# Performance work log

Measured on AMD Instinct MI355X. Metric: run time of the kernel, lower is better.

Reference implementation:

```python
import jax, jax.numpy as jnp
import numpy as np

VAR0, VAR1 = 0.1, 0.2          # SSD variances
IOU_THRESH = 0.5
NUM_CLASSES = 21
NEGPOS_RATIO = 3
ALPHA = 1.0


def mid_to_corner(b):
    # [cx,cy,w,h] -> [xmin,ymin,xmax,ymax]
    return jnp.concatenate([b[:, :2] - b[:, 2:] / 2, b[:, :2] + b[:, 2:] / 2], axis=1)


def jaccard(box_a, box_b):
    # box_a [n,4], box_b [P,4] corner form -> IoU [n,P]
    lt = jnp.maximum(box_a[:, None, :2], box_b[None, :, :2])
    rb = jnp.minimum(box_a[:, None, 2:], box_b[None, :, 2:])
    wh = jnp.clip(rb - lt, 0.0)
    inter = wh[..., 0] * wh[..., 1]
    area_a = (box_a[:, 2] - box_a[:, 0]) * (box_a[:, 3] - box_a[:, 1])
    area_b = (box_b[:, 2] - box_b[:, 0]) * (box_b[:, 3] - box_b[:, 1])
    union = area_a[:, None] + area_b[None, :] - inter
    return inter / union


def encode_offset(matched, priors):
    # matched corner form [P,4], priors center form [P,4]
    g_cxcy = ((matched[:, :2] + matched[:, 2:]) / 2 - priors[:, :2]) / (VAR0 * priors[:, 2:])
    g_wh = jnp.log((matched[:, 2:] - matched[:, :2]) / priors[:, 2:]) / VAR1
    return jnp.concatenate([g_cxcy, g_wh], axis=1)


def match_one(gt_box, gt_cls, valid, priors_corner, priors_mid):
    # gt_box [n,4], gt_cls [n], valid [n] bool; priors [P,4]
    n = gt_box.shape[0]
    P = priors_corner.shape[0]
    ovl = jaccard(gt_box, priors_corner)                    # [n,P]
    ovl = jnp.where(valid[:, None], ovl, -1.0)              # mask padded GTs
    best_truth_idx = jnp.argmax(ovl, axis=0)                # [P]
    best_truth_ovl = jnp.max(ovl, axis=0)                   # [P]
    best_prior_idx = jnp.argmax(ovl, axis=1)                # [n]
    bpi = jnp.where(valid, best_prior_idx, P)               # OOB for padded -> dropped
    best_truth_ovl = best_truth_ovl.at[bpi].set(2.0, mode='drop')
    best_truth_idx = best_truth_idx.at[bpi].set(jnp.arange(n), mode='drop')
    matches = gt_box[best_truth_idx]                        # [P,4]
    loc = encode_offset(matches, priors_mid)                # [P,4]
    conf = gt_cls[best_truth_idx].astype(jnp.int32) + 1     # [P]
    conf = jnp.where(best_truth_ovl < IOU_THRESH, 0, conf)
    return loc, conf


def setup_inputs() -> dict:
    key = jax.random.key(0)
    k = jax.random.split(key, 8)
    B, P, C, NMAX = 64, 8732, 21, 50
    confidence = jax.random.normal(k[0], (B, P, C), dtype=jnp.float32)
    location = 0.1 * jax.random.normal(k[1], (B, P, 4), dtype=jnp.float32)
    cxcy = jax.random.uniform(k[2], (P, 2), minval=0.05, maxval=0.95)
    pwh = jax.random.uniform(k[3], (P, 2), minval=0.05, maxval=0.4)
    prior_boxes = jnp.concatenate([cxcy, pwh], axis=1).astype(jnp.float32)
    xymin = jax.random.uniform(k[4], (B, NMAX, 2), minval=0.0, maxval=0.6)
    gwh = jax.random.uniform(k[5], (B, NMAX, 2), minval=0.05, maxval=0.35)
    cls = jax.random.randint(k[6], (B, NMAX), 0, C - 1).astype(jnp.float32)
    labels = jnp.concatenate([xymin, xymin + gwh, cls[..., None]], axis=-1).astype(jnp.float32)
    obj_count = jax.random.randint(k[7], (B, 1), 1, NMAX + 1).astype(jnp.int32)
    return {"confidence": confidence, "location": location,
            "prior_boxes": prior_boxes, "labels": labels, "obj_count": obj_count}


def reference(confidence, location, prior_boxes, labels, obj_count):
    B, P, C = confidence.shape
    NMAX = labels.shape[1]
    priors_corner = mid_to_corner(prior_boxes)
    valid = jnp.arange(NMAX)[None, :] < obj_count            # [B,NMAX]
    loc_t, conf_t = jax.vmap(match_one, in_axes=(0, 0, 0, None, None))(
        labels[..., :4], labels[..., 4], valid, priors_corner, prior_boxes)
    # loc_t [B,P,4] float, conf_t [B,P] int32

    pos = conf_t > 0                                          # [B,P]
    # smooth-L1 over positive anchors (sum reduction)
    d = jnp.abs(location - loc_t)
    sl1 = jnp.where(d < 1.0, 0.5 * d * d, d - 0.5)
    loss_loc = jnp.sum(sl1 * pos[..., None].astype(sl1.dtype))

    # hard negative mining score: global-max logsumexp minus target logit
    bc = confidence.reshape(-1, C)
    x_max = jnp.max(bc)
    lse = jnp.log(jnp.sum(jnp.exp(bc - x_max), axis=1)) + x_max
    tgt_logit = jnp.take_along_axis(bc, conf_t.reshape(-1, 1), axis=1)[:, 0]
    loss_c = (lse - tgt_logit).reshape(B, P)
    loss_c = jnp.where(pos, 0.0, loss_c)
    loss_idx = jnp.argsort(-loss_c, axis=1)                   # descending sort
    idx_rank = jnp.argsort(loss_idx, axis=1)
    num_pos = jnp.sum(pos.astype(jnp.int32), axis=1, keepdims=True)   # [B,1]
    num_neg = jnp.clip(NEGPOS_RATIO * num_pos, None, P - 1)
    neg = idx_rank < num_neg                                  # [B,P]

    # standard cross entropy over selected (pos|neg) anchors, sum reduction
    logp = jax.nn.log_softmax(confidence, axis=-1)            # [B,P,C]
    nll = -jnp.take_along_axis(logp, conf_t[..., None], axis=-1)[..., 0]
    sel = jnp.logical_or(pos, neg)
    loss_conf = jnp.sum(nll * sel.astype(nll.dtype))

    N = jnp.sum(num_pos).astype(confidence.dtype)
    return (ALPHA * loss_loc / N, loss_conf / N)
```

## Files before the change

### kernel.cpp

```cpp
#include <hip/hip_runtime.h>
#include <math.h>

#define Bn 64
#define Pn 8732
#define Cn 21
#define NMAXn 50
#define PX 35

template <int C>
__device__ __forceinline__ float dppf(float x) {
    return __int_as_float(__builtin_amdgcn_update_dpp(0, __float_as_int(x), C, 0xf, 0xf, true));
}
template <int C>
__device__ __forceinline__ int dppi(int x) {
    return __builtin_amdgcn_update_dpp(0, x, C, 0xf, 0xf, true);
}
__device__ __forceinline__ float wave_sum_f(float x) {
    x += dppf<0x111>(x); x += dppf<0x112>(x); x += dppf<0x114>(x);
    x += dppf<0x118>(x); x += dppf<0x142>(x); x += dppf<0x143>(x);
    return x;
}
__device__ __forceinline__ int wave_sum_i(int x) {
    x += dppi<0x111>(x); x += dppi<0x112>(x); x += dppi<0x114>(x);
    x += dppi<0x118>(x); x += dppi<0x142>(x); x += dppi<0x143>(x);
    return x;
}

__device__ __forceinline__ float smoothl1_enc(const float4 l, const float4 pr,
                                              float gx0, float gy0, float gx1, float gy1) {
    const float tx = ((gx0 + gx1) * 0.5f - pr.x) / (0.1f * pr.z);
    const float ty = ((gy0 + gy1) * 0.5f - pr.y) / (0.1f * pr.w);
    const float tw = __logf((gx1 - gx0) / pr.z) * 5.0f;
    const float th = __logf((gy1 - gy0) / pr.w) * 5.0f;
    float s = 0.0f, d;
    d = fabsf(l.x - tx); s += (d < 1.0f) ? 0.5f * d * d : d - 0.5f;
    d = fabsf(l.y - ty); s += (d < 1.0f) ? 0.5f * d * d : d - 0.5f;
    d = fabsf(l.z - tw); s += (d < 1.0f) ? 0.5f * d * d : d - 0.5f;
    d = fabsf(l.w - th); s += (d < 1.0f) ? 0.5f * d * d : d - 0.5f;
    return s;
}

__global__ __launch_bounds__(256) void k_fused(const float* __restrict__ conf,
                                               const float* __restrict__ loc,
                                               const float* __restrict__ priors,
                                               const float* __restrict__ labels,
                                               const int* __restrict__ objc,
                                               float* __restrict__ lc,
                                               float* __restrict__ part_loc,
                                               float* __restrict__ part_nll,
                                               int* __restrict__ part_np,
                                               int* __restrict__ sbp_g) {
    const int bx = blockIdx.x;
    const int tid = threadIdx.x;
    const int lane = tid & 63, wid = tid >> 6;

    __shared__ float sconf[256 * Cn];
    __shared__ float lab[NMAXn * 5];
    __shared__ float rl[4], rn[4];
    __shared__ int rp[4];
    __shared__ float wkI[4], wkU[4];
    __shared__ int wkP[4];

    if (bx < Bn * PX) {
        const int b = bx / PX;
        const int px = bx % PX;
        const int p0 = px * 256;
        const int rows = min(256, Pn - p0);
        const int cnt = objc[b];
        const float* lb = labels + b * NMAXn * 5;

        const float4* src = reinterpret_cast<const float4*>(conf + ((size_t)b * Pn + p0) * Cn);
        const int n4 = rows * Cn / 4;
        for (int i = tid; i < n4; i += 256) reinterpret_cast<float4*>(sconf)[i] = src[i];
        for (int i = tid; i < NMAXn * 5; i += 256) lab[i] = labels[b * NMAXn * 5 + i];

        const int p = p0 + tid;
        const int pcl = (p < Pn) ? p : (Pn - 1);
        const float4 pr = reinterpret_cast<const float4*>(priors)[pcl];
        const float px0 = pr.x - 0.5f * pr.z, py0 = pr.y - 0.5f * pr.w;
        const float px1 = pr.x + 0.5f * pr.z, py1 = pr.y + 0.5f * pr.w;
        const float parea = (px1 - px0) * (py1 - py0);
        float bI = 0.0f, bU = 1.0f;
        int bidx = 0;
        {
            const float gx0 = lb[0], gy0 = lb[1], gx1 = lb[2], gy1 = lb[3];
            const float lx = fmaxf(gx0, px0), ly = fmaxf(gy0, py0);
            const float rx = fminf(gx1, px1), ry = fminf(gy1, py1);
            const float w = fmaxf(rx - lx, 0.0f), h = fmaxf(ry - ly, 0.0f);
            bI = w * h;
            bU = (gx1 - gx0) * (gy1 - gy0) + parea - bI;
        }
        for (int n = 1; n < cnt; ++n) {
            const float gx0 = lb[n * 5 + 0], gy0 = lb[n * 5 + 1];
            const float gx1 = lb[n * 5 + 2], gy1 = lb[n * 5 + 3];
            const float lx = fmaxf(gx0, px0), ly = fmaxf(gy0, py0);
            const float rx = fminf(gx1, px1), ry = fminf(gy1, py1);
            const float w = fmaxf(rx - lx, 0.0f), h = fmaxf(ry - ly, 0.0f);
            const float I = w * h;
            const float U = (gx1 - gx0) * (gy1 - gy0) + parea - I;
            if (I * bU > bI * U) { bI = I; bU = U; bidx = n; }
        }
        __syncthreads();

        float my_loc = 0.0f, my_nll = 0.0f;
        int my_np = 0;
        if (tid < rows) {
            const size_t gi = (size_t)b * Pn + p;
            const int ct = (2.0f * bI >= bU) ? ((int)lab[bidx * 5 + 4] + 1) : 0;
            const float* row = sconf + tid * Cn;
            float m = row[0];
#pragma unroll
            for (int j = 1; j < Cn; ++j) m = fmaxf(m, row[j]);
            float s2 = 0.0f;
#pragma unroll
            for (int j = 0; j < Cn; ++j) s2 += __expf(row[j] - m);
            const float nll = __logf(s2) + m - row[ct];
            if (ct > 0) {
                lc[gi] = 0.0f;
                my_np = 1;
                my_nll = nll;
                const float4 l = reinterpret_cast<const float4*>(loc)[gi];
                my_loc = smoothl1_enc(l, pr, lab[bidx * 5 + 0], lab[bidx * 5 + 1],
                                      lab[bidx * 5 + 2], lab[bidx * 5 + 3]);
            } else {
                lc[gi] = nll;
            }
        }
        my_loc = wave_sum_f(my_loc);
        my_nll = wave_sum_f(my_nll);
        my_np = wave_sum_i(my_np);
        if (lane == 63) { rl[wid] = my_loc; rn[wid] = my_nll; rp[wid] = my_np; }
        __syncthreads();
        if (tid == 0) {
            const int g = b * PX + px;
            part_loc[g] = rl[0] + rl[1] + rl[2] + rl[3];
            part_nll[g] = rn[0] + rn[1] + rn[2] + rn[3];
            part_np[g] = rp[0] + rp[1] + rp[2] + rp[3];
        }
    } else {
        const int idx = bx - Bn * PX;
        const int b = idx / NMAXn;
        const int n = idx % NMAXn;
        if (n >= objc[b]) return;
        const float* lbp = labels + (b * NMAXn + n) * 5;
        const float gx0 = lbp[0], gy0 = lbp[1], gx1 = lbp[2], gy1 = lbp[3];
        const float ga = (gx1 - gx0) * (gy1 - gy0);
        float bI, bU;
        int bp_;
        {
            const float4 pr = reinterpret_cast<const float4*>(priors)[tid];
            const float px0 = pr.x - 0.5f * pr.z, py0 = pr.y - 0.5f * pr.w;
            const float px1 = pr.x + 0.5f * pr.z, py1 = pr.y + 0.5f * pr.w;
            const float lx = fmaxf(gx0, px0), ly = fmaxf(gy0, py0);
            const float rx = fminf(gx1, px1), ry = fminf(gy1, py1);
            const float w = fmaxf(rx - lx, 0.0f), h = fmaxf(ry - ly, 0.0f);
            bI = w * h;
            bU = ga + (px1 - px0) * (py1 - py0) - bI;
            bp_ = tid;
        }
        for (int j = 1; j < PX; ++j) {
            const int p = tid + 256 * j;
            if (p < Pn) {
                const float4 pr = reinterpret_cast<const float4*>(priors)[p];
                const float px0 = pr.x - 0.5f * pr.z, py0 = pr.y - 0.5f * pr.w;
                const float px1 = pr.x + 0.5f * pr.z, py1 = pr.y + 0.5f * pr.w;
                const float lx = fmaxf(gx0, px0), ly = fmaxf(gy0, py0);
                const float rx = fminf(gx1, px1), ry = fminf(gy1, py1);
                const float w = fmaxf(rx - lx, 0.0f), h = fmaxf(ry - ly, 0.0f);
                const float I = w * h;
                const float U = ga + (px1 - px0) * (py1 - py0) - I;
                if (I * bU > bI * U) { bI = I; bU = U; bp_ = p; }
            }
        }
        for (int off = 32; off > 0; off >>= 1) {
            const float oI = __shfl_down(bI, off);
            const float oU = __shfl_down(bU, off);
            const int op = __shfl_down(bp_, off);
            const float a = oI * bU, c = bI * oU;
            if (a > c || (a == c && op < bp_)) { bI = oI; bU = oU; bp_ = op; }
        }
        if (lane == 0) { wkI[wid] = bI; wkU[wid] = bU; wkP[wid] = bp_; }
        __syncthreads();
        if (tid == 0) {
            float cI = wkI[0], cU = wkU[0];
            int cp = wkP[0];
#pragma unroll
            for (int w = 1; w < 4; ++w) {
                const float a = wkI[w] * cU, c = cI * wkU[w];
                if (a > c || (a == c && wkP[w] < cp)) { cI = wkI[w]; cU = wkU[w]; cp = wkP[w]; }
            }
            sbp_g[b * NMAXn + n] = cp;
        }
    }
}

__global__ __launch_bounds__(64) void k_fix(const float* __restrict__ conf,
                                            const float* __restrict__ loc,
                                            const float* __restrict__ priors,
                                            const float* __restrict__ labels,
                                            const int* __restrict__ objc,
                                            const int* __restrict__ sbp_g,
                                            float* __restrict__ lc,
                                            int* __restrict__ fix_np,
                                            float* __restrict__ fix_nll,
                                            float* __restrict__ fix_loc,
                                            int* __restrict__ done) {
    __shared__ int sbp[NMAXn];
    __shared__ float lab[NMAXn * 5];
    const int b = blockIdx.x;
    const int tid = threadIdx.x;
    if (b == 0 && tid == 0) *done = 0;
    const int cnt = objc[b];
    for (int i = tid; i < NMAXn * 5; i += 64) lab[i] = labels[b * NMAXn * 5 + i];
    if (tid < cnt) sbp[tid] = sbp_g[b * NMAXn + tid];
    __syncthreads();
    bool win = false;
    if (tid < cnt) {
        const int myp = sbp[tid];
        win = true;
        for (int n2 = tid + 1; n2 < cnt; ++n2) win = win && (sbp[n2] != myp);
    }
    float dnll = 0.0f, dloc = 0.0f;
    int dnp = 0;
    if (win) {
        const int pp = sbp[tid];
        const float4 prf = reinterpret_cast<const float4*>(priors)[pp];
        const float qx0 = prf.x - 0.5f * prf.z, qy0 = prf.y - 0.5f * prf.w;
        const float qx1 = prf.x + 0.5f * prf.z, qy1 = prf.y + 0.5f * prf.w;
        const float qarea = (qx1 - qx0) * (qy1 - qy0);
        float bI = 0.0f, bU = 1.0f;
        int bidx2 = 0;
        {
            const float gx0 = lab[0], gy0 = lab[1], gx1 = lab[2], gy1 = lab[3];
            const float lx = fmaxf(gx0, qx0), ly = fmaxf(gy0, qy0);
            const float rx = fminf(gx1, qx1), ry = fminf(gy1, qy1);
            const float w = fmaxf(rx - lx, 0.0f), h = fmaxf(ry - ly, 0.0f);
            bI = w * h;
            bU = (gx1 - gx0) * (gy1 - gy0) + qarea - bI;
        }
        for (int n2 = 1; n2 < cnt; ++n2) {
            const float gx0 = lab[n2 * 5 + 0], gy0 = lab[n2 * 5 + 1];
            const float gx1 = lab[n2 * 5 + 2], gy1 = lab[n2 * 5 + 3];
            const float lx = fmaxf(gx0, qx0), ly = fmaxf(gy0, qy0);
            const float rx = fminf(gx1, qx1), ry = fminf(gy1, qy1);
            const float w = fmaxf(rx - lx, 0.0f), h = fmaxf(ry - ly, 0.0f);
            const float I = w * h;
            const float U = (gx1 - gx0) * (gy1 - gy0) + qarea - I;
            if (I * bU > bI * U) { bI = I; bU = U; bidx2 = n2; }
        }
        const float* rowg = conf + ((size_t)b * Pn + pp) * Cn;
        float m2 = rowg[0];
#pragma unroll
        for (int j = 1; j < Cn; ++j) m2 = fmaxf(m2, rowg[j]);
        float ss = 0.0f;
#pragma unroll
        for (int j = 0; j < Cn; ++j) ss += __expf(rowg[j] - m2);
        const float lse = __logf(ss) + m2;
        const int ctn = (int)lab[tid * 5 + 4] + 1;
        const float4 lv = reinterpret_cast<const float4*>(loc)[(size_t)b * Pn + pp];
        dnll = lse - rowg[ctn];
        dloc = smoothl1_enc(lv, prf, lab[tid * 5 + 0], lab[tid * 5 + 1],
                            lab[tid * 5 + 2], lab[tid * 5 + 3]);
        dnp = 1;
        if (2.0f * bI >= bU) {
            const int cto = (int)lab[bidx2 * 5 + 4] + 1;
            dnll -= (lse - rowg[cto]);
            dloc -= smoothl1_enc(lv, prf, lab[bidx2 * 5 + 0], lab[bidx2 * 5 + 1],
                                 lab[bidx2 * 5 + 2], lab[bidx2 * 5 + 3]);
            dnp = 0;
        }
        lc[(size_t)b * Pn + pp] = 0.0f;
    }
    dnll = wave_sum_f(dnll);
    dloc = wave_sum_f(dloc);
    dnp = wave_sum_i(dnp);
    if (tid == 63) {
        fix_nll[b] = dnll;
        fix_loc[b] = dloc;
        fix_np[b] = dnp;
    }
}

__global__ __launch_bounds__(256) void k_neg(const float* __restrict__ lc,
                                             const float* __restrict__ part_loc,
                                             const float* __restrict__ part_nll,
                                             const int* __restrict__ part_np,
                                             const int* __restrict__ fix_np,
                                             const float* __restrict__ fix_nll,
                                             const float* __restrict__ fix_loc,
                                             float* __restrict__ negsum,
                                             int* __restrict__ done,
                                             float* __restrict__ out) {
    const int b = blockIdx.x;
    const int tid = threadIdx.x;
    const int lane = tid & 63, wid = tid >> 6;
    __shared__ int redc[2][4];
    __shared__ float redf[4], redf2[4];
    __shared__ int redi[4];
    __shared__ int np_sh, islast;

    const int NV = Pn / 4;
    const float4* src = reinterpret_cast<const float4*>(lc + (size_t)b * Pn);
    const float4 sent = make_float4(-1.0f, -1.0f, -1.0f, -1.0f);
    float4 rr[12];
#pragma unroll
    for (int j = 0; j < 12; ++j) {
        const int i = tid + 256 * j;
        rr[j] = (i < NV) ? src[i] : sent;
    }

    if (tid < 64) {
        int npl = (tid < PX) ? part_np[b * PX + tid] : 0;
        npl = wave_sum_i(npl);
        if (tid == 63) np_sh = npl;
    }
    __syncthreads();
    const int k = min(3 * (np_sh + fix_np[b]), Pn - 1);

    unsigned lo = 0u, hi = 0x7F800000u;
#pragma unroll 1
    for (int it = 0; it < 31; ++it) {
        const unsigned mid = lo + ((hi - lo) >> 1);
        const float fm = __uint_as_float(mid);
        int c = 0;
#pragma unroll
        for (int j = 0; j < 12; ++j)
            c += (rr[j].x >= fm) + (rr[j].y >= fm) + (rr[j].z >= fm) + (rr[j].w >= fm);
        c = wave_sum_i(c);
        if (lane == 63) redc[it & 1][wid] = c;
        __syncthreads();
        const int tot = redc[it & 1][0] + redc[it & 1][1]
                      + redc[it & 1][2] + redc[it & 1][3];
        if (tot >= k) lo = mid;
        else hi = mid;
    }
    const float v = __uint_as_float(lo);

    float sm = 0.0f;
    int c = 0;
#pragma unroll
    for (int j = 0; j < 12; ++j) {
        if (rr[j].x > v) { sm += rr[j].x; ++c; }
        if (rr[j].y > v) { sm += rr[j].y; ++c; }
        if (rr[j].z > v) { sm += rr[j].z; ++c; }
        if (rr[j].w > v) { sm += rr[j].w; ++c; }
    }
    sm = wave_sum_f(sm);
    c = wave_sum_i(c);
    if (lane == 63) { redf[wid] = sm; redi[wid] = c; }
    __syncthreads();
    if (tid == 0) {
        const float st = redf[0] + redf[1] + redf[2] + redf[3];
        const int ct = redi[0] + redi[1] + redi[2] + redi[3];
        negsum[b] = st + (float)(k - ct) * v;
        __threadfence();
        islast = (atomicAdd(done, 1) == Bn - 1) ? 1 : 0;
    }
    __syncthreads();
    if (!islast) return;
    __threadfence();

    float sl = 0.0f, sn = 0.0f;
    int np = 0;
    for (int i = tid; i < Bn * PX; i += 256) {
        sl += part_loc[i];
        sn += part_nll[i];
        np += part_np[i];
    }
    if (tid < Bn) {
        sn += negsum[tid] + fix_nll[tid];
        sl += fix_loc[tid];
        np += fix_np[tid];
    }
    sl = wave_sum_f(sl);
    sn = wave_sum_f(sn);
    np = wave_sum_i(np);
    if (lane == 63) { redf[wid] = sn; redf2[wid] = sl; redi[wid] = np; }
    __syncthreads();
    if (tid == 0) {
        const float fN = (float)(redi[0] + redi[1] + redi[2] + redi[3]);
        out[0] = (redf2[0] + redf2[1] + redf2[2] + redf2[3]) / fN;
        out[1] = (redf[0] + redf[1] + redf[2] + redf[3]) / fN;
    }
}

extern "C" void kernel_launch(void* const* d_in, const int* in_sizes, int n_in,
                              void* d_out, int out_size, void* d_ws, size_t ws_size,
                              hipStream_t stream) {
    const float* conf = (const float*)d_in[0];
    const float* loc = (const float*)d_in[1];
    const float* priors = (const float*)d_in[2];
    const float* labels = (const float*)d_in[3];
    const int* objc = (const int*)d_in[4];
    float* out = (float*)d_out;

    int* sbp_g = (int*)d_ws;
    float* part_loc = (float*)(sbp_g + Bn * NMAXn);
    float* part_nll = part_loc + Bn * PX;
    int* part_np = (int*)(part_nll + Bn * PX);
    float* negsum = (float*)(part_np + Bn * PX);
    int* fix_np = (int*)(negsum + Bn);
    float* fix_nll = (float*)(fix_np + Bn);
    float* fix_loc = fix_nll + Bn;
    float* lc = fix_loc + Bn;
    int* done = (int*)(lc + (size_t)Bn * Pn);

    k_fused<<<Bn * PX + Bn * NMAXn, 256, 0, stream>>>(conf, loc, priors, labels, objc,
                                                      lc, part_loc, part_nll, part_np,
                                                      sbp_g);
    k_fix<<<Bn, 64, 0, stream>>>(conf, loc, priors, labels, objc, sbp_g, lc,
                                 fix_np, fix_nll, fix_loc, done);
    k_neg<<<Bn, 256, 0, stream>>>(lc, part_loc, part_nll, part_np,
                                  fix_np, fix_nll, fix_loc, negsum, done, out);
}
```

Measured before the change: 70.29 us.

## Fuse forced-match fixup into negative-mining kernel and dual-accumulate IoU argmax loops

Removes the separate k_fix launch by running the forced-match correction inside the negative-mining kernel. The corrected prior indices are applied to register-held loss values instead of being written back to global memory. Both IoU argmax loops in the main kernel now keep two independent running maxima to shorten the dependency chain, then merge them with an index tie-break. The done-counter reset moves into the first kernel. This saves one launch and a global round trip, but adds serial fixup work before the bisection in each block.

```diff
diff --git a/kernel.cpp b/kernel.cpp
--- a/kernel.cpp
+++ b/kernel.cpp
@@ -40,6 +40,15 @@
     return s;
 }
 
+#define IOU_IU(gx0, gy0, gx1, gy1, qx0, qy0, qx1, qy1, qarea, I, U)            \
+    {                                                                          \
+        const float lx = fmaxf(gx0, qx0), ly = fmaxf(gy0, qy0);                \
+        const float rx = fminf(gx1, qx1), ry = fminf(gy1, qy1);                \
+        const float w = fmaxf(rx - lx, 0.0f), h = fmaxf(ry - ly, 0.0f);        \
+        I = w * h;                                                             \
+        U = (gx1 - gx0) * (gy1 - gy0) + qarea - I;                             \
+    }
+
 __global__ __launch_bounds__(256) void k_fused(const float* __restrict__ conf,
                                                const float* __restrict__ loc,
                                                const float* __restrict__ priors,
@@ -49,10 +58,12 @@
                                                float* __restrict__ part_loc,
                                                float* __restrict__ part_nll,
                                                int* __restrict__ part_np,
-                                               int* __restrict__ sbp_g) {
+                                               int* __restrict__ sbp_g,
+                                               int* __restrict__ done) {
     const int bx = blockIdx.x;
     const int tid = threadIdx.x;
     const int lane = tid & 63, wid = tid >> 6;
+    if (bx == 0 && tid == 0) *done = 0;
 
     __shared__ float sconf[256 * Cn];
     __shared__ float lab[NMAXn * 5];
@@ -80,25 +91,27 @@
         const float px0 = pr.x - 0.5f * pr.z, py0 = pr.y - 0.5f * pr.w;
         const float px1 = pr.x + 0.5f * pr.z, py1 = pr.y + 0.5f * pr.w;
         const float parea = (px1 - px0) * (py1 - py0);
-        float bI = 0.0f, bU = 1.0f;
-        int bidx = 0;
+        float bI0 = 0.0f, bU0 = 1.0f, bI1 = 0.0f, bU1 = 1.0f;
+        int bx0 = 0, bx1 = 0;
+        int n = 0;
+        for (; n + 1 < cnt; n += 2) {
+            float I0, U0, I1, U1;
+            IOU_IU(lb[n * 5 + 0], lb[n * 5 + 1], lb[n * 5 + 2], lb[n * 5 + 3],
+                   px0, py0, px1, py1, parea, I0, U0);
+            IOU_IU(lb[(n + 1) * 5 + 0], lb[(n + 1) * 5 + 1], lb[(n + 1) * 5 + 2],
+                   lb[(n + 1) * 5 + 3], px0, py0, px1, py1, parea, I1, U1);
+            if (I0 * bU0 > bI0 * U0) { bI0 = I0; bU0 = U0; bx0 = n; }
+            if (I1 * bU1 > bI1 * U1) { bI1 = I1; bU1 = U1; bx1 = n + 1; }
+        }
+        if (n < cnt) {
+            float I0, U0;
+            IOU_IU(lb[n * 5 + 0], lb[n * 5 + 1], lb[n * 5 + 2], lb[n * 5 + 3],
+                   px0, py0, px1, py1, parea, I0, U0);
+            if (I0 * bU0 > bI0 * U0) { bI0 = I0; bU0 = U0; bx0 = n; }
+        }
         {
-            const float gx0 = lb[0], gy0 = lb[1], gx1 = lb[2], gy1 = lb[3];
-            const float lx = fmaxf(gx0, px0), ly = fmaxf(gy0, py0);
-            const float rx = fminf(gx1, px1), ry = fminf(gy1, py1);
-            const float w = fmaxf(rx - lx, 0.0f), h = fmaxf(ry - ly, 0.0f);
-            bI = w * h;
-            bU = (gx1 - gx0) * (gy1 - gy0) + parea - bI;
-        }
-        for (int n = 1; n < cnt; ++n) {
-            const float gx0 = lb[n * 5 + 0], gy0 = lb[n * 5 + 1];
-            const float gx1 = lb[n * 5 + 2], gy1 = lb[n * 5 + 3];
-            const float lx = fmaxf(gx0, px0), ly = fmaxf(gy0, py0);
-            const float rx = fminf(gx1, px1), ry = fminf(gy1, py1);
-            const float w = fmaxf(rx - lx, 0.0f), h = fmaxf(ry - ly, 0.0f);
-            const float I = w * h;
-            const float U = (gx1 - gx0) * (gy1 - gy0) + parea - I;
-            if (I * bU > bI * U) { bI = I; bU = U; bidx = n; }
+            const float a = bI1 * bU0, c = bI0 * bU1;
+            if (a > c || (a == c && bx1 < bx0)) { bI0 = bI1; bU0 = bU1; bx0 = bx1; }
         }
         __syncthreads();
 
@@ -106,7 +119,7 @@
         int my_np = 0;
         if (tid < rows) {
             const size_t gi = (size_t)b * Pn + p;
-            const int ct = (2.0f * bI >= bU) ? ((int)lab[bidx * 5 + 4] + 1) : 0;
+            const int ct = (2.0f * bI0 >= bU0) ? ((int)lab[bx0 * 5 + 4] + 1) : 0;
             const float* row = sconf + tid * Cn;
             float m = row[0];
 #pragma unroll
@@ -120,8 +133,8 @@
                 my_np = 1;
                 my_nll = nll;
                 const float4 l = reinterpret_cast<const float4*>(loc)[gi];
-                my_loc = smoothl1_enc(l, pr, lab[bidx * 5 + 0], lab[bidx * 5 + 1],
-                                      lab[bidx * 5 + 2], lab[bidx * 5 + 3]);
+                my_loc = smoothl1_enc(l, pr, lab[bx0 * 5 + 0], lab[bx0 * 5 + 1],
+                                      lab[bx0 * 5 + 2], lab[bx0 * 5 + 3]);
             } else {
                 lc[gi] = nll;
             }
@@ -144,42 +157,69 @@
         if (n >= objc[b]) return;
         const float* lbp = labels + (b * NMAXn + n) * 5;
         const float gx0 = lbp[0], gy0 = lbp[1], gx1 = lbp[2], gy1 = lbp[3];
-        const float ga = (gx1 - gx0) * (gy1 - gy0);
-        float bI, bU;
-        int bp_;
+        float bI0, bU0, bI1, bU1;
+        int bp0, bp1;
         {
             const float4 pr = reinterpret_cast<const float4*>(priors)[tid];
-            const float px0 = pr.x - 0.5f * pr.z, py0 = pr.y - 0.5f * pr.w;
-            const float px1 = pr.x + 0.5f * pr.z, py1 = pr.y + 0.5f * pr.w;
-            const float lx = fmaxf(gx0, px0), ly = fmaxf(gy0, py0);
-            const float rx = fminf(gx1, px1), ry = fminf(gy1, py1);
-            const float w = fmaxf(rx - lx, 0.0f), h = fmaxf(ry - ly, 0.0f);
-            bI = w * h;
-            bU = ga + (px1 - px0) * (py1 - py0) - bI;
-            bp_ = tid;
-        }
-        for (int j = 1; j < PX; ++j) {
-            const int p = tid + 256 * j;
-            if (p < Pn) {
-                const float4 pr = reinterpret_cast<const float4*>(priors)[p];
-                const float px0 = pr.x - 0.5f * pr.z, py0 = pr.y - 0.5f * pr.w;
-                const float px1 = pr.x + 0.5f * pr.z, py1 = pr.y + 0.5f * pr.w;
-                const float lx = fmaxf(gx0, px0), ly = fmaxf(gy0, py0);
-                const float rx = fminf(gx1, px1), ry = fminf(gy1, py1);
-                const float w = fmaxf(rx - lx, 0.0f), h = fmaxf(ry - ly, 0.0f);
-                const float I = w * h;
-                const float U = ga + (px1 - px0) * (py1 - py0) - I;
-                if (I * bU > bI * U) { bI = I; bU = U; bp_ = p; }
-            }
+            const float qx0 = pr.x - 0.5f * pr.z, qy0 = pr.y - 0.5f * pr.w;
+            const float qx1 = pr.x + 0.5f * pr.z, qy1 = pr.y + 0.5f * pr.w;
+            IOU_IU(gx0, gy0, gx1, gy1, qx0, qy0, qx1, qy1,
+                   (qx1 - qx0) * (qy1 - qy0), bI0, bU0);
+            bp0 = tid;
+        }
+        {
+            const float4 pr = reinterpret_cast<const float4*>(priors)[tid + 256];
+            const float qx0 = pr.x - 0.5f * pr.z, qy0 = pr.y - 0.5f * pr.w;
+            const float qx1 = pr.x + 0.5f * pr.z, qy1 = pr.y + 0.5f * pr.w;
+            IOU_IU(gx0, gy0, gx1, gy1, qx0, qy0, qx1, qy1,
+                   (qx1 - qx0) * (qy1 - qy0), bI1, bU1);
+            bp1 = tid + 256;
+        }
+        int j = 2;
+        for (; j + 1 < PX; j += 2) {
+            const int pA = tid + 256 * j, pB = pA + 256;
+            float IA, UA, IB, UB;
+            {
+                const float4 pr = reinterpret_cast<const float4*>(priors)[pA];
+                const float qx0 = pr.x - 0.5f * pr.z, qy0 = pr.y - 0.5f * pr.w;
+                const float qx1 = pr.x + 0.5f * pr.z, qy1 = pr.y + 0.5f * pr.w;
+                IOU_IU(gx0, gy0, gx1, gy1, qx0, qy0, qx1, qy1,
+                       (qx1 - qx0) * (qy1 - qy0), IA, UA);
+            }
+            {
+                const float4 pr = reinterpret_cast<const float4*>(priors)[pB];
+                const float qx0 = pr.x - 0.5f * pr.z, qy0 = pr.y - 0.5f * pr.w;
+                const float qx1 = pr.x + 0.5f * pr.z, qy1 = pr.y + 0.5f * pr.w;
+                IOU_IU(gx0, gy0, gx1, gy1, qx0, qy0, qx1, qy1,
+                       (qx1 - qx0) * (qy1 - qy0), IB, UB);
+            }
+            if (IA * bU0 > bI0 * UA) { bI0 = IA; bU0 = UA; bp0 = pA; }
+            if (IB * bU1 > bI1 * UB) { bI1 = IB; bU1 = UB; bp1 = pB; }
+        }
+        {
+            const int pA = tid + 256 * 34;
+            if (pA < Pn) {
+                const float4 pr = reinterpret_cast<const float4*>(priors)[pA];
+                const float qx0 = pr.x - 0.5f * pr.z, qy0 = pr.y - 0.5f * pr.w;
+                const float qx1 = pr.x + 0.5f * pr.z, qy1 = pr.y + 0.5f * pr.w;
+                float IA, UA;
+                IOU_IU(gx0, gy0, gx1, gy1, qx0, qy0, qx1, qy1,
+                       (qx1 - qx0) * (qy1 - qy0), IA, UA);
+                if (IA * bU0 > bI0 * UA) { bI0 = IA; bU0 = UA; bp0 = pA; }
+            }
+        }
+        {
+            const float a = bI1 * bU0, c = bI0 * bU1;
+            if (a > c || (a == c && bp1 < bp0)) { bI0 = bI1; bU0 = bU1; bp0 = bp1; }
         }
         for (int off = 32; off > 0; off >>= 1) {
-            const float oI = __shfl_down(bI, off);
-            const float oU = __shfl_down(bU, off);
-            const int op = __shfl_down(bp_, off);
-            const float a = oI * bU, c = bI * oU;
-            if (a > c || (a == c && op < bp_)) { bI = oI; bU = oU; bp_ = op; }
-        }
-        if (lane == 0) { wkI[wid] = bI; wkU[wid] = bU; wkP[wid] = bp_; }
+            const float oI = __shfl_down(bI0, off);
+            const float oU = __shfl_down(bU0, off);
+            const int op = __shfl_down(bp0, off);
+            const float a = oI * bU0, c = bI0 * oU;
+            if (a > c || (a == c && op < bp0)) { bI0 = oI; bU0 = oU; bp0 = op; }
+        }
+        if (lane == 0) { wkI[wid] = bI0; wkU[wid] = bU0; wkP[wid] = bp0; }
         __syncthreads();
         if (tid == 0) {
             float cI = wkI[0], cU = wkU[0];
@@ -194,106 +234,29 @@
     }
 }
 
-__global__ __launch_bounds__(64) void k_fix(const float* __restrict__ conf,
-                                            const float* __restrict__ loc,
-                                            const float* __restrict__ priors,
-                                            const float* __restrict__ labels,
-                                            const int* __restrict__ objc,
-                                            const int* __restrict__ sbp_g,
-                                            float* __restrict__ lc,
-                                            int* __restrict__ fix_np,
-                                            float* __restrict__ fix_nll,
-                                            float* __restrict__ fix_loc,
-                                            int* __restrict__ done) {
-    __shared__ int sbp[NMAXn];
-    __shared__ float lab[NMAXn * 5];
-    const int b = blockIdx.x;
-    const int tid = threadIdx.x;
-    if (b == 0 && tid == 0) *done = 0;
-    const int cnt = objc[b];
-    for (int i = tid; i < NMAXn * 5; i += 64) lab[i] = labels[b * NMAXn * 5 + i];
-    if (tid < cnt) sbp[tid] = sbp_g[b * NMAXn + tid];
-    __syncthreads();
-    bool win = false;
-    if (tid < cnt) {
-        const int myp = sbp[tid];
-        win = true;
-        for (int n2 = tid + 1; n2 < cnt; ++n2) win = win && (sbp[n2] != myp);
-    }
-    float dnll = 0.0f, dloc = 0.0f;
-    int dnp = 0;
-    if (win) {
-        const int pp = sbp[tid];
-        const float4 prf = reinterpret_cast<const float4*>(priors)[pp];
-        const float qx0 = prf.x - 0.5f * prf.z, qy0 = prf.y - 0.5f * prf.w;
-        const float qx1 = prf.x + 0.5f * prf.z, qy1 = prf.y + 0.5f * prf.w;
-        const float qarea = (qx1 - qx0) * (qy1 - qy0);
-        float bI = 0.0f, bU = 1.0f;
-        int bidx2 = 0;
-        {
-            const float gx0 = lab[0], gy0 = lab[1], gx1 = lab[2], gy1 = lab[3];
-            const float lx = fmaxf(gx0, qx0), ly = fmaxf(gy0, qy0);
-            const float rx = fminf(gx1, qx1), ry = fminf(gy1, qy1);
-            const float w = fmaxf(rx - lx, 0.0f), h = fmaxf(ry - ly, 0.0f);
-            bI = w * h;
-            bU = (gx1 - gx0) * (gy1 - gy0) + qarea - bI;
-        }
-        for (int n2 = 1; n2 < cnt; ++n2) {
-            const float gx0 = lab[n2 * 5 + 0], gy0 = lab[n2 * 5 + 1];
-            const float gx1 = lab[n2 * 5 + 2], gy1 = lab[n2 * 5 + 3];
-            const float lx = fmaxf(gx0, qx0), ly = fmaxf(gy0, qy0);
-            const float rx = fminf(gx1, qx1), ry = fminf(gy1, qy1);
-            const float w = fmaxf(rx - lx, 0.0f), h = fmaxf(ry - ly, 0.0f);
-            const float I = w * h;
-            const float U = (gx1 - gx0) * (gy1 - gy0) + qarea - I;
-            if (I * bU > bI * U) { bI = I; bU = U; bidx2 = n2; }
-        }
-        const float* rowg = conf + ((size_t)b * Pn + pp) * Cn;
-        float m2 = rowg[0];
-#pragma unroll
-        for (int j = 1; j < Cn; ++j) m2 = fmaxf(m2, rowg[j]);
-        float ss = 0.0f;
-#pragma unroll
-        for (int j = 0; j < Cn; ++j) ss += __expf(rowg[j] - m2);
-        const float lse = __logf(ss) + m2;
-        const int ctn = (int)lab[tid * 5 + 4] + 1;
-        const float4 lv = reinterpret_cast<const float4*>(loc)[(size_t)b * Pn + pp];
-        dnll = lse - rowg[ctn];
-        dloc = smoothl1_enc(lv, prf, lab[tid * 5 + 0], lab[tid * 5 + 1],
-                            lab[tid * 5 + 2], lab[tid * 5 + 3]);
-        dnp = 1;
-        if (2.0f * bI >= bU) {
-            const int cto = (int)lab[bidx2 * 5 + 4] + 1;
-            dnll -= (lse - rowg[cto]);
-            dloc -= smoothl1_enc(lv, prf, lab[bidx2 * 5 + 0], lab[bidx2 * 5 + 1],
-                                 lab[bidx2 * 5 + 2], lab[bidx2 * 5 + 3]);
-            dnp = 0;
-        }
-        lc[(size_t)b * Pn + pp] = 0.0f;
-    }
-    dnll = wave_sum_f(dnll);
-    dloc = wave_sum_f(dloc);
-    dnp = wave_sum_i(dnp);
-    if (tid == 63) {
-        fix_nll[b] = dnll;
-        fix_loc[b] = dloc;
-        fix_np[b] = dnp;
-    }
-}
-
-__global__ __launch_bounds__(256) void k_neg(const float* __restrict__ lc,
-                                             const float* __restrict__ part_loc,
-                                             const float* __restrict__ part_nll,
-                                             const int* __restrict__ part_np,
-                                             const int* __restrict__ fix_np,
-                                             const float* __restrict__ fix_nll,
-                                             const float* __restrict__ fix_loc,
-                                             float* __restrict__ negsum,
-                                             int* __restrict__ done,
-                                             float* __restrict__ out) {
+__global__ __launch_bounds__(256) void k_negfix(const float* __restrict__ conf,
+                                                const float* __restrict__ loc,
+                                                const float* __restrict__ priors,
+                                                const float* __restrict__ labels,
+                                                const int* __restrict__ objc,
+                                                const int* __restrict__ sbp_g,
+                                                const float* __restrict__ lc,
+                                                const float* __restrict__ part_loc,
+                                                const float* __restrict__ part_nll,
+                                                const int* __restrict__ part_np,
+                                                int* __restrict__ fix_np,
+                                                float* __restrict__ fix_nll,
+                                                float* __restrict__ fix_loc,
+                                                float* __restrict__ negsum,
+                                                int* __restrict__ done,
+                                                float* __restrict__ out) {
     const int b = blockIdx.x;
     const int tid = threadIdx.x;
     const int lane = tid & 63, wid = tid >> 6;
+    __shared__ float lab[NMAXn * 5];
+    __shared__ int sbp[NMAXn];
+    __shared__ int flist[NMAXn];
+    __shared__ int fcnt_s, dnp_s;
     __shared__ int redc[2][4];
     __shared__ float redf[4], redf2[4];
     __shared__ int redi[4];
@@ -309,13 +272,94 @@
         rr[j] = (i < NV) ? src[i] : sent;
     }
 
+    const int cnt = objc[b];
     if (tid < 64) {
-        int npl = (tid < PX) ? part_np[b * PX + tid] : 0;
+        for (int i = tid; i < NMAXn * 5; i += 64) lab[i] = labels[b * NMAXn * 5 + i];
+        if (tid < cnt) sbp[tid] = sbp_g[b * NMAXn + tid];
+    } else if (tid < 128) {
+        const int t = tid - 64;
+        int npl = (t < PX) ? part_np[b * PX + t] : 0;
         npl = wave_sum_i(npl);
-        if (tid == 63) np_sh = npl;
+        if (t == 63) np_sh = npl;
     }
     __syncthreads();
-    const int k = min(3 * (np_sh + fix_np[b]), Pn - 1);
+
+    if (tid < 64) {
+        bool win = false;
+        if (tid < cnt) {
+            const int myp = sbp[tid];
+            win = true;
+            for (int n2 = tid + 1; n2 < cnt; ++n2) win = win && (sbp[n2] != myp);
+        }
+        const unsigned long long wmask = __ballot(win);
+        float dnll = 0.0f, dloc = 0.0f;
+        int dnp = 0;
+        if (win) {
+            const int pp = sbp[tid];
+            const float4 prf = reinterpret_cast<const float4*>(priors)[pp];
+            const float qx0 = prf.x - 0.5f * prf.z, qy0 = prf.y - 0.5f * prf.w;
+            const float qx1 = prf.x + 0.5f * prf.z, qy1 = prf.y + 0.5f * prf.w;
+            const float qarea = (qx1 - qx0) * (qy1 - qy0);
+            float bI = 0.0f, bU = 1.0f;
+            int bidx2 = 0;
+            for (int n2 = 0; n2 < cnt; ++n2) {
+                float I, U;
+                IOU_IU(lab[n2 * 5 + 0], lab[n2 * 5 + 1], lab[n2 * 5 + 2],
+                       lab[n2 * 5 + 3], qx0, qy0, qx1, qy1, qarea, I, U);
+                if (I * bU > bI * U) { bI = I; bU = U; bidx2 = n2; }
+            }
+            const float* rowg = conf + ((size_t)b * Pn + pp) * Cn;
+            float m2 = rowg[0];
+#pragma unroll
+            for (int j = 1; j < Cn; ++j) m2 = fmaxf(m2, rowg[j]);
+            float ss = 0.0f;
+#pragma unroll
+            for (int j = 0; j < Cn; ++j) ss += __expf(rowg[j] - m2);
+            const float lse = __logf(ss) + m2;
+            const int ctn = (int)lab[tid * 5 + 4] + 1;
+            const float4 lv = reinterpret_cast<const float4*>(loc)[(size_t)b * Pn + pp];
+            dnll = lse - rowg[ctn];
+            dloc = smoothl1_enc(lv, prf, lab[tid * 5 + 0], lab[tid * 5 + 1],
+                                lab[tid * 5 + 2], lab[tid * 5 + 3]);
+            dnp = 1;
+            if (2.0f * bI >= bU) {
+                const int cto = (int)lab[bidx2 * 5 + 4] + 1;
+                dnll -= (lse - rowg[cto]);
+                dloc -= smoothl1_enc(lv, prf, lab[bidx2 * 5 + 0], lab[bidx2 * 5 + 1],
+                                     lab[bidx2 * 5 + 2], lab[bidx2 * 5 + 3]);
+                dnp = 0;
+            }
+            const int sidx = __popcll(wmask & ((1ull << lane) - 1));
+            flist[sidx] = pp;
+        }
+        dnll = wave_sum_f(dnll);
+        dloc = wave_sum_f(dloc);
+        dnp = wave_sum_i(dnp);
+        if (tid == 63) {
+            fix_nll[b] = dnll;
+            fix_loc[b] = dloc;
+            fix_np[b] = dnp;
+            dnp_s = dnp;
+            fcnt_s = (int)__popcll(wmask);
+        }
+    }
+    __syncthreads();
+
+    const int fcnt = fcnt_s;
+    for (int i = 0; i < fcnt; ++i) {
+        const int pp = flist[i];
+#pragma unroll
+        for (int j = 0; j < 12; ++j) {
+            const int base = (tid + 256 * j) << 2;
+            if (pp >= base && pp < base + 4) {
+                if (pp == base) rr[j].x = 0.0f;
+                else if (pp == base + 1) rr[j].y = 0.0f;
+                else if (pp == base + 2) rr[j].z = 0.0f;
+                else rr[j].w = 0.0f;
+            }
+        }
+    }
+    const int k = min(3 * (np_sh + dnp_s), Pn - 1);
 
     unsigned lo = 0u, hi = 0x7F800000u;
 #pragma unroll 1
@@ -407,9 +451,8 @@
 
     k_fused<<<Bn * PX + Bn * NMAXn, 256, 0, stream>>>(conf, loc, priors, labels, objc,
                                                       lc, part_loc, part_nll, part_np,
-                                                      sbp_g);
-    k_fix<<<Bn, 64, 0, stream>>>(conf, loc, priors, labels, objc, sbp_g, lc,
-                                 fix_np, fix_nll, fix_loc, done);
-    k_neg<<<Bn, 256, 0, stream>>>(lc, part_loc, part_nll, part_np,
-                                  fix_np, fix_nll, fix_loc, negsum, done, out);
-}
+                                                      sbp_g, done);
+    k_negfix<<<Bn, 256, 0, stream>>>(conf, loc, priors, labels, objc, sbp_g, lc,
+                                     part_loc, part_nll, part_np,
+                                     fix_np, fix_nll, fix_loc, negsum, done, out);
+}
```

After: 84.71 us. +20.5%, slower.
